# Performance work log

Hardware: AMD Instinct MI355X
Metric: run time of the kernel (lower is better)

The kernel has to match this reference:

```python
import jax, jax.numpy as jnp
import numpy as np

MHC_ITERS = 5  # init kwarg mhc_iters


def setup_inputs() -> dict:
    key = jax.random.key(0)
    # (batch, seq, n_lanes, n_lanes) lane-mixing logits
    x = jax.random.normal(key, (2048, 1024, 8, 8), dtype=jnp.float32)
    return {"x": x}


def reference(x):
    input_dtype = x.dtype
    shape = x.shape
    n = shape[-1]
    # flatten leading dims -> (B, n, n), compute in fp32 (autocast disabled in original)
    M = jnp.exp(x.reshape(-1, n, n).astype(jnp.float32))
    # Sinkhorn-Knopp: alternate row / column normalization
    for _ in range(MHC_ITERS):
        M = M / jnp.sum(M, axis=-1, keepdims=True)  # row normalize
        M = M / jnp.sum(M, axis=-2, keepdims=True)  # col normalize
    return M.reshape(shape).astype(input_dtype)
```

## Files before the change

### kernel.cpp

```cpp
#include <hip/hip_runtime.h>


constexpr int MHC_ITERS = 5;
constexpr int THREADS = 128;
constexpr int F4_PER_BLOCK = THREADS * 16;

__global__ __launch_bounds__(THREADS)
void fused_mhc_kernel(const float* __restrict__ x,
                      float* __restrict__ out,
                      int nmat) {
    __shared__ float4 lds[F4_PER_BLOCK];

    const int t = threadIdx.x;
    const size_t mat0 = (size_t)blockIdx.x * THREADS;
    const float4* __restrict__ src = reinterpret_cast<const float4*>(x) + mat0 * 16;
    float4* __restrict__ dst = reinterpret_cast<float4*>(out) + mat0 * 16;

    #pragma unroll
    for (int p = 0; p < 16; ++p) {
        int g = p * THREADS + t;
        int s = g ^ ((g >> 4) & 15);
        lds[s] = src[g];
    }
    __syncthreads();

    float M[64];
    const int mlow = t & 15;
    #pragma unroll
    for (int k = 0; k < 16; ++k) {
        float4 v = lds[t * 16 + (k ^ mlow)];
        M[k * 4 + 0] = v.x;
        M[k * 4 + 1] = v.y;
        M[k * 4 + 2] = v.z;
        M[k * 4 + 3] = v.w;
    }

    #pragma unroll
    for (int i = 0; i < 64; ++i) M[i] = __expf(M[i]);

    #pragma unroll
    for (int it = 0; it < MHC_ITERS; ++it) {
        #pragma unroll
        for (int r = 0; r < 8; ++r) {
            float s = 0.0f;
            #pragma unroll
            for (int c = 0; c < 8; ++c) s += M[r * 8 + c];
            float inv = __builtin_amdgcn_rcpf(s);
            #pragma unroll
            for (int c = 0; c < 8; ++c) M[r * 8 + c] *= inv;
        }
        #pragma unroll
        for (int c = 0; c < 8; ++c) {
            float s = 0.0f;
            #pragma unroll
            for (int r = 0; r < 8; ++r) s += M[r * 8 + c];
            float inv = __builtin_amdgcn_rcpf(s);
            #pragma unroll
            for (int r = 0; r < 8; ++r) M[r * 8 + c] *= inv;
        }
    }

    #pragma unroll
    for (int k = 0; k < 16; ++k) {
        float4 v;
        v.x = M[k * 4 + 0];
        v.y = M[k * 4 + 1];
        v.z = M[k * 4 + 2];
        v.w = M[k * 4 + 3];
        lds[t * 16 + (k ^ mlow)] = v;
    }
    __syncthreads();

    #pragma unroll
    for (int p = 0; p < 16; ++p) {
        int g = p * THREADS + t;
        int s = g ^ ((g >> 4) & 15);
        dst[g] = lds[s];
    }
}

extern "C" void kernel_launch(void* const* d_in, const int* in_sizes, int n_in,
                              void* d_out, int out_size, void* d_ws, size_t ws_size,
                              hipStream_t stream) {
    const float* x = (const float*)d_in[0];
    float* out = (float*)d_out;

    const int nmat = in_sizes[0] / 64;
    const int blocks = nmat / THREADS;

    fused_mhc_kernel<<<blocks, THREADS, 0, stream>>>(x, out, nmat);
}
```

Before: 205.9 us.

## Split each 8x8 matrix across four lanes with DPP quad reductions

Instead of one thread holding a whole 8x8 matrix in 64 registers, four threads each hold two rows, and column sums are combined across the quad with DPP xor-shuffles. Blocks grow to 256 threads covering 64 matrices. The aim is to cut register pressure so more waves can be resident and memory latency is better hidden. In exchange each column step adds cross-lane DPP operations, and the block uses more threads per matrix.

```diff
diff --git a/kernel.cpp b/kernel.cpp
--- a/kernel.cpp
+++ b/kernel.cpp
@@ -2,46 +2,53 @@
 
 
 constexpr int MHC_ITERS = 5;
-constexpr int THREADS = 128;
-constexpr int F4_PER_BLOCK = THREADS * 16;
+constexpr int THREADS = 256;
+constexpr int MATS_PER_BLOCK = THREADS / 4;
+constexpr int F4_PER_BLOCK = MATS_PER_BLOCK * 16;
+
+template <int CTRL>
+__device__ __forceinline__ float quad_xor_add(float x) {
+    int peer = __builtin_amdgcn_update_dpp(0, __float_as_int(x), CTRL, 0xF, 0xF, true);
+    return x + __int_as_float(peer);
+}
 
 __global__ __launch_bounds__(THREADS)
-void fused_mhc_kernel(const float* __restrict__ x,
-                      float* __restrict__ out,
-                      int nmat) {
+void fused_mhc_kernel(const float* __restrict__ x, float* __restrict__ out) {
     __shared__ float4 lds[F4_PER_BLOCK];
 
     const int t = threadIdx.x;
-    const size_t mat0 = (size_t)blockIdx.x * THREADS;
-    const float4* __restrict__ src = reinterpret_cast<const float4*>(x) + mat0 * 16;
-    float4* __restrict__ dst = reinterpret_cast<float4*>(out) + mat0 * 16;
+    const size_t base = (size_t)blockIdx.x * F4_PER_BLOCK;
+    const float4* __restrict__ src = reinterpret_cast<const float4*>(x) + base;
+    float4* __restrict__ dst = reinterpret_cast<float4*>(out) + base;
 
     #pragma unroll
-    for (int p = 0; p < 16; ++p) {
+    for (int p = 0; p < 4; ++p) {
         int g = p * THREADS + t;
-        int s = g ^ ((g >> 4) & 15);
-        lds[s] = src[g];
+        lds[g ^ ((g >> 4) & 15)] = src[g];
     }
     __syncthreads();
 
-    float M[64];
-    const int mlow = t & 15;
+    const int m = t >> 2;
+    const int h = t & 3;
+    const int swz = m & 15;
+
+    float M[16];
     #pragma unroll
-    for (int k = 0; k < 16; ++k) {
-        float4 v = lds[t * 16 + (k ^ mlow)];
-        M[k * 4 + 0] = v.x;
-        M[k * 4 + 1] = v.y;
-        M[k * 4 + 2] = v.z;
-        M[k * 4 + 3] = v.w;
+    for (int j = 0; j < 4; ++j) {
+        float4 v = lds[(m * 16 + h * 4 + j) ^ swz];
+        M[j * 4 + 0] = v.x;
+        M[j * 4 + 1] = v.y;
+        M[j * 4 + 2] = v.z;
+        M[j * 4 + 3] = v.w;
     }
 
     #pragma unroll
-    for (int i = 0; i < 64; ++i) M[i] = __expf(M[i]);
+    for (int i = 0; i < 16; ++i) M[i] = __expf(M[i]);
 
     #pragma unroll
     for (int it = 0; it < MHC_ITERS; ++it) {
         #pragma unroll
-        for (int r = 0; r < 8; ++r) {
+        for (int r = 0; r < 2; ++r) {
             float s = 0.0f;
             #pragma unroll
             for (int c = 0; c < 8; ++c) s += M[r * 8 + c];
@@ -51,31 +58,30 @@
         }
         #pragma unroll
         for (int c = 0; c < 8; ++c) {
-            float s = 0.0f;
-            #pragma unroll
-            for (int r = 0; r < 8; ++r) s += M[r * 8 + c];
-            float inv = __builtin_amdgcn_rcpf(s);
-            #pragma unroll
-            for (int r = 0; r < 8; ++r) M[r * 8 + c] *= inv;
+            float part = M[c] + M[8 + c];
+            part = quad_xor_add<0xB1>(part);
+            part = quad_xor_add<0x4E>(part);
+            float inv = __builtin_amdgcn_rcpf(part);
+            M[c] *= inv;
+            M[8 + c] *= inv;
         }
     }
 
     #pragma unroll
-    for (int k = 0; k < 16; ++k) {
+    for (int j = 0; j < 4; ++j) {
         float4 v;
-        v.x = M[k * 4 + 0];
-        v.y = M[k * 4 + 1];
-        v.z = M[k * 4 + 2];
-        v.w = M[k * 4 + 3];
-        lds[t * 16 + (k ^ mlow)] = v;
+        v.x = M[j * 4 + 0];
+        v.y = M[j * 4 + 1];
+        v.z = M[j * 4 + 2];
+        v.w = M[j * 4 + 3];
+        lds[(m * 16 + h * 4 + j) ^ swz] = v;
     }
     __syncthreads();
 
     #pragma unroll
-    for (int p = 0; p < 16; ++p) {
+    for (int p = 0; p < 4; ++p) {
         int g = p * THREADS + t;
-        int s = g ^ ((g >> 4) & 15);
-        dst[g] = lds[s];
+        dst[g] = lds[g ^ ((g >> 4) & 15)];
     }
 }
 
@@ -86,7 +92,7 @@
     float* out = (float*)d_out;
 
     const int nmat = in_sizes[0] / 64;
-    const int blocks = nmat / THREADS;
+    const int blocks = nmat / MATS_PER_BLOCK;
 
-    fused_mhc_kernel<<<blocks, THREADS, 0, stream>>>(x, out, nmat);
+    fused_mhc_kernel<<<blocks, THREADS, 0, stream>>>(x, out);
 }
```

Result: faster. 190.2 us (-7.6%).
